# Kernel optimization log

Hardware: AMD Instinct MI355X
Metric: run time of the kernel (lower is better)

The kernel has to match this reference:

```python
import jax, jax.numpy as jnp
import numpy as np

N_QUBITS = 14
N_LOCAL = 3
VQC_DEPTH = 6
BATCH = 512
NLOC = 2 ** N_LOCAL            # 8 = Hermitian dimension
NOFF = NLOC * (NLOC - 1) // 2  # 28 off-diagonal params
_ROWS, _COLS = np.tril_indices(NLOC, -1)  # row-major order matches the torch nested loop


def _make_hermitian(a, b, d):
    # Faithful to create_Hermitian: h[i,j]=A[k]+iB[k] for j<i (row-major over i=1..N-1),
    # h[i-1,i-1]=D[i] for i=1..N-1 (D[0] unused, last diag 0), then H = h + h^H.
    tri = jnp.zeros((NLOC, NLOC), jnp.complex64).at[_ROWS, _COLS].set(a + 1j * b)
    diag = jnp.concatenate([d[1:], jnp.zeros(1, d.dtype)]).astype(jnp.complex64)
    h = tri + jnp.diag(diag)
    return h + h.conj().T


def _apply_ry(state, angle, wire):
    # state: (B, 2, 2, ..., 2); angle: scalar (shared) or (B,) per-sample
    half = 0.5 * angle
    c, s = jnp.cos(half), jnp.sin(half)
    if jnp.ndim(angle) == 1:
        bshape = (angle.shape[0],) + (1,) * (N_QUBITS - 1)
        c, s = c.reshape(bshape), s.reshape(bshape)
    s0 = jnp.take(state, 0, axis=wire + 1)
    s1 = jnp.take(state, 1, axis=wire + 1)
    return jnp.stack([c * s0 - s * s1, s * s0 + c * s1], axis=wire + 1)


def _apply_cnot(state, ctrl):
    # CNOT with target = ctrl + 1 (the only pattern used by entangling_layer)
    ax = ctrl + 1
    s0 = jnp.take(state, 0, axis=ax)
    s1 = jnp.take(state, 1, axis=ax)
    # after removing the control axis, the target axis sits at position ax
    s1 = jnp.flip(s1, axis=ax)
    return jnp.stack([s0, s1], axis=ax)


def _circuit(X, theta, H):
    B = X.shape[0]
    # Hadamard layer applied to |0...0> yields the uniform superposition
    amp = 1.0 / np.sqrt(2.0 ** N_QUBITS)
    state = jnp.full((B,) + (2,) * N_QUBITS, amp, dtype=jnp.complex64)
    for w in range(N_QUBITS):
        state = _apply_ry(state, X[:, w], w)
    for k in range(VQC_DEPTH):
        for i in range(0, N_QUBITS - 1, 2):
            state = _apply_cnot(state, i)
        for i in range(1, N_QUBITS - 1, 2):
            state = _apply_cnot(state, i)
        for w in range(N_QUBITS):
            state = _apply_ry(state, theta[k, w], w)
    exps = []
    for q in range(N_QUBITS):
        wires = [(q + j) % N_QUBITS for j in range(N_LOCAL)]
        psi = jnp.moveaxis(state, [w + 1 for w in wires], list(range(1, N_LOCAL + 1)))
        psi = psi.reshape(B, NLOC, -1)  # (B, 8, 2^(n-3))
        e = jnp.einsum('bir,ij,bjr->b', psi.conj(), H[q], psi).real
        exps.append(e)
    return jnp.stack(exps, axis=1).astype(jnp.float32)  # (B, n_qubits)


def setup_inputs() -> dict:
    key = jax.random.key(0)
    k = jax.random.split(key, 5)
    X = jax.random.normal(k[0], (BATCH, N_QUBITS), jnp.float32)
    theta = 0.01 * jax.random.normal(k[1], (VQC_DEPTH, N_QUBITS), jnp.float32)
    A = 2.0 * jax.random.normal(k[2], (N_QUBITS, NOFF), jnp.float32)
    Bp = 2.0 * jax.random.normal(k[3], (N_QUBITS, NOFF), jnp.float32)
    D = 2.0 * jax.random.normal(k[4], (N_QUBITS, NLOC), jnp.float32)
    return {"X": X, "theta": theta, "A": A, "B": Bp, "D": D}


def reference(X, theta, A, B, D):
    H = jax.vmap(_make_hermitian)(A, B, D)  # (n_qubits, 8, 8) complex64
    q_out = _circuit(X, theta, H)
    return q_out[:, :2]
```

## Files before the change

kernel.cpp:

```cpp
#include <hip/hip_runtime.h>
#include <math.h>

#define NQ 14
#define NSTATE (1 << 14)
#define DEPTH  6
#define NT     1024

typedef float v2f __attribute__((ext_vector_type(2)));

__device__ __forceinline__ int swz(int n) { return n ^ ((n >> 4) & 28); }

__device__ __forceinline__ int sigma(int n) {
    int m = n ^ ((n & 0x1554) >> 1);
    return m ^ ((m & 0x2AAA) >> 1);
}

__device__ __forceinline__ v2f pkmul_cc(v2f a, v2f cs) {
    v2f d;
    asm("v_pk_mul_f32 %0, %1, %2 op_sel:[0,0] op_sel_hi:[1,0]"
        : "=v"(d) : "v"(a), "v"(cs));
    return d;
}
__device__ __forceinline__ v2f pkmul_ss(v2f a, v2f cs) {
    v2f d;
    asm("v_pk_mul_f32 %0, %1, %2 op_sel:[0,1] op_sel_hi:[1,1]"
        : "=v"(d) : "v"(a), "v"(cs));
    return d;
}
__device__ __forceinline__ v2f pkfma_cc(v2f a, v2f cs, v2f acc) {
    v2f d;
    asm("v_pk_fma_f32 %0, %1, %2, %3 op_sel:[0,0,0] op_sel_hi:[1,0,1]"
        : "=v"(d) : "v"(a), "v"(cs), "v"(acc));
    return d;
}
__device__ __forceinline__ v2f pkfma_nss(v2f a, v2f cs, v2f acc) {
    v2f d;
    asm("v_pk_fma_f32 %0, %1, %2, %3 op_sel:[0,1,0] op_sel_hi:[1,1,1] neg_lo:[0,1,0] neg_hi:[0,1,0]"
        : "=v"(d) : "v"(a), "v"(cs), "v"(acc));
    return d;
}
__device__ __forceinline__ v2f pkfma_sw(v2f a, v2f cs, v2f acc) {
    v2f d;
    asm("v_pk_fma_f32 %0, %1, %2, %3 op_sel:[1,1,0] op_sel_hi:[0,1,1] neg_lo:[0,1,0] neg_hi:[0,0,0]"
        : "=v"(d) : "v"(a), "v"(cs), "v"(acc));
    return d;
}
__device__ __forceinline__ v2f pkfma(v2f a, v2f bb, v2f acc) {
    v2f d;
    asm("v_pk_fma_f32 %0, %1, %2, %3"
        : "=v"(d) : "v"(a), "v"(bb), "v"(acc));
    return d;
}

__device__ __forceinline__ void ry_pk0(float (&p)[16], v2f cs) {
#pragma unroll
    for (int j = 0; j < 8; ++j) {
        v2f v = *(v2f*)&p[2 * j];
        *(v2f*)&p[2 * j] = pkfma_sw(v, cs, pkmul_cc(v, cs));
    }
}
template <int JB>
__device__ __forceinline__ void ry_pkN(float (&p)[16], v2f cs) {
#pragma unroll
    for (int j = 0; j < 8; ++j) {
        if (!((j >> (JB - 1)) & 1)) {
            const int j1 = j | (1 << (JB - 1));
            v2f a0 = *(v2f*)&p[2 * j], a1 = *(v2f*)&p[2 * j1];
            *(v2f*)&p[2 * j]  = pkfma_nss(a1, cs, pkmul_cc(a0, cs));
            *(v2f*)&p[2 * j1] = pkfma_cc(a1, cs, pkmul_ss(a0, cs));
        }
    }
}
__device__ __forceinline__ void ry4_pk(float (&p)[16], float2 q0, float2 q1,
                                       float2 q2, float2 q3) {
    v2f c0, c1, c2, c3;
    c0.x = q0.x; c0.y = q0.y;
    c1.x = q1.x; c1.y = q1.y;
    c2.x = q2.x; c2.y = q2.y;
    c3.x = q3.x; c3.y = q3.y;
    ry_pk0(p, c0);
    ry_pkN<1>(p, c1);
    ry_pkN<2>(p, c2);
    ry_pkN<3>(p, c3);
}

template <int CTRL>
__device__ __forceinline__ void ry_dpp_pk(float (&p)[16], float c, float sg) {
    v2f cs; cs.x = c; cs.y = 0.0f;
    v2f sgv; sgv.x = sg; sgv.y = sg;
#pragma unroll
    for (int j = 0; j < 8; ++j) {
        v2f pt;
        pt.x = __int_as_float(__builtin_amdgcn_update_dpp(
            0, __float_as_int(p[2 * j]), CTRL, 0xF, 0xF, true));
        pt.y = __int_as_float(__builtin_amdgcn_update_dpp(
            0, __float_as_int(p[2 * j + 1]), CTRL, 0xF, 0xF, true));
        v2f v = *(v2f*)&p[2 * j];
        *(v2f*)&p[2 * j] = pkfma(pt, sgv, pkmul_cc(v, cs));
    }
}

template <int C1, int C2>
__device__ __forceinline__ void ry_dpp2_pk(float (&p)[16], float c, float sg) {
    v2f cs; cs.x = c; cs.y = 0.0f;
    v2f sgv; sgv.x = sg; sgv.y = sg;
#pragma unroll
    for (int j = 0; j < 8; ++j) {
        v2f pt;
        int ax = __builtin_amdgcn_update_dpp(
            0, __float_as_int(p[2 * j]), C1, 0xF, 0xF, true);
        pt.x = __int_as_float(__builtin_amdgcn_update_dpp(
            0, ax, C2, 0xF, 0xF, true));
        int ay = __builtin_amdgcn_update_dpp(
            0, __float_as_int(p[2 * j + 1]), C1, 0xF, 0xF, true);
        pt.y = __int_as_float(__builtin_amdgcn_update_dpp(
            0, ay, C2, 0xF, 0xF, true));
        v2f v = *(v2f*)&p[2 * j];
        *(v2f*)&p[2 * j] = pkfma(pt, sgv, pkmul_cc(v, cs));
    }
}

__global__ __launch_bounds__(NT, 4)
void vqc_kernel(const float* __restrict__ X,
                const float* __restrict__ TH,
                const float* __restrict__ A,
                const float* __restrict__ Bc,
                const float* __restrict__ D,
                float* __restrict__ out)
{
    __shared__ __align__(16) float st[NSTATE];
    __shared__ float2 tb[DEPTH * NQ];
    __shared__ float2 xf[NQ];
    __shared__ float  red[2 * (NT / 64)];

    const int t = threadIdx.x;
    const int b = blockIdx.x;

    if (t < DEPTH * NQ) {
        float s, c;
        __sincosf(0.5f * TH[t], &s, &c);
        tb[t] = make_float2(c, s);
    } else if (t < DEPTH * NQ + NQ) {
        const int j = t - DEPTH * NQ;
        float s, c;
        __sincosf(0.5f * X[b * NQ + (13 - j)], &s, &c);
        xf[j] = make_float2(c - s, c + s);
    }
    __syncthreads();

    {
        const int mt = sigma(t << 4);
        float sh = 1.0f / 128.0f;
#pragma unroll
        for (int j = 4; j < 14; ++j) {
            float2 f = xf[j];
            sh *= ((mt >> j) & 1) ? f.y : f.x;
        }
        float fa[4], fb[4];
#pragma unroll
        for (int j = 0; j < 4; ++j) {
            float2 f = xf[j];
            const int mj = (mt >> j) & 1;
            fa[j] = mj ? f.y : f.x;
            fb[j] = mj ? f.x : f.y;
        }
        float p[16];
#pragma unroll
        for (int i = 0; i < 16; ++i) {
            const int sl = sigma(i);
            float v = sh;
            v *= (sl & 1)        ? fb[0] : fa[0];
            v *= ((sl >> 1) & 1) ? fb[1] : fa[1];
            v *= ((sl >> 2) & 1) ? fb[2] : fa[2];
            v *= ((sl >> 3) & 1) ? fb[3] : fa[3];
            p[i] = v;
        }
        ry4_pk(p, tb[13], tb[12], tb[11], tb[10]);
        float2 w9 = tb[9], w8 = tb[8];
        const float sg9 = (t & 1) ? w9.y : -w9.y;
        const float sg8 = (t & 2) ? w8.y : -w8.y;
        ry_dpp_pk<0xB1>(p, w9.x, sg9);
        ry_dpp_pk<0x4E>(p, w8.x, sg8);
        const int wb = swz(t << 4);
#pragma unroll
        for (int g = 0; g < 4; ++g)
            *(float4*)&st[wb ^ (g << 2)] =
                make_float4(p[4 * g], p[4 * g + 1], p[4 * g + 2], p[4 * g + 3]);
    }
    __syncthreads();

    for (int k = 0; k < DEPTH; ++k) {
        const float2* tbk = tb + k * NQ;

        if (k > 0) {
            const int rb = swz(sigma(t << 4) & ~15) ^ ((t & 1) * 12);
            float tmpf[16];
#pragma unroll
            for (int g = 0; g < 4; ++g)
                *(float4*)&tmpf[g * 4] = *(const float4*)&st[rb ^ (g << 2)];
            float p[16];
#pragma unroll
            for (int i = 0; i < 16; ++i) {
                const int i0 = i & 1, i1 = (i >> 1) & 1, i2 = (i >> 2) & 1, i3 = (i >> 3) & 1;
                const int s = (i0 ^ i1 ^ i2) | ((i1 ^ i2) << 1) | ((i2 ^ i3) << 2) | (i3 << 3);
                p[i] = tmpf[s];
            }
            __syncthreads();
            ry4_pk(p, tbk[13], tbk[12], tbk[11], tbk[10]);
            float2 w9 = tbk[9], w8 = tbk[8];
            const float sg9 = (t & 1) ? w9.y : -w9.y;
            const float sg8 = (t & 2) ? w8.y : -w8.y;
            ry_dpp_pk<0xB1>(p, w9.x, sg9);
            ry_dpp_pk<0x4E>(p, w8.x, sg8);
            const int wb = swz(t << 4);
#pragma unroll
            for (int g = 0; g < 4; ++g)
                *(float4*)&st[wb ^ (g << 2)] =
                    make_float4(p[4 * g], p[4 * g + 1], p[4 * g + 2], p[4 * g + 3]);
            __syncthreads();
        }

        {
            const int raw = ((t >> 4) & 3) | (((t >> 6) & 15) << 2)
                          | ((t & 3) << 6) | (((t >> 2) & 3) << 8);
            const int base2 = swz(raw);
            float p[16];
#pragma unroll
            for (int i = 0; i < 16; ++i) p[i] = st[base2 + (i << 10)];
            ry4_pk(p, tbk[3], tbk[2], tbk[1], tbk[0]);
            float2 w7 = tbk[7], w6 = tbk[6], w5 = tbk[5], w4 = tbk[4];
            const float sg7 = (t & 1) ? w7.y : -w7.y;
            const float sg6 = (t & 2) ? w6.y : -w6.y;
            const float sg5 = (t & 4) ? w5.y : -w5.y;
            const float sg4 = (t & 8) ? w4.y : -w4.y;
            ry_dpp_pk<0xB1>(p, w7.x, sg7);
            ry_dpp_pk<0x4E>(p, w6.x, sg6);
            ry_dpp2_pk<0x1B, 0x141>(p, w5.x, sg5);
            ry_dpp2_pk<0x141, 0x140>(p, w4.x, sg4);
#pragma unroll
            for (int i = 0; i < 16; ++i) st[base2 + (i << 10)] = p[i];
            __syncthreads();
        }
    }

    float e[2];
#pragma unroll
    for (int q = 0; q < 2; ++q) {
        const int shift = 11 - q;
        float dg[8];
#pragma unroll
        for (int i = 0; i < 7; ++i) dg[i] = 2.0f * D[q * 8 + i + 1];
        dg[7] = 0.0f;
        float acc = 0.0f;
        const int lowmask = (1 << shift) - 1;
        for (int r = t; r < NSTATE / 8; r += NT) {
            const int base = ((r >> shift) << (shift + 3)) | (r & lowmask);
            float ps[8];
#pragma unroll
            for (int i = 0; i < 8; ++i) ps[i] = st[swz(base + (i << shift))];
#pragma unroll
            for (int i = 0; i < 8; ++i) acc += dg[i] * ps[i] * ps[i];
            int kk = 0;
#pragma unroll
            for (int i = 1; i < 8; ++i)
#pragma unroll
                for (int j = 0; j < i; ++j, ++kk)
                    acc += 2.0f * A[q * 28 + kk] * ps[i] * ps[j];
        }
        e[q] = acc;
    }

    float v0 = e[0], v1 = e[1];
#pragma unroll
    for (int o = 32; o > 0; o >>= 1) {
        v0 += __shfl_down(v0, o);
        v1 += __shfl_down(v1, o);
    }
    if ((t & 63) == 0) {
        red[(t >> 6) * 2]     = v0;
        red[(t >> 6) * 2 + 1] = v1;
    }
    __syncthreads();
    if (t == 0) {
        float s0 = 0.0f, s1 = 0.0f;
#pragma unroll
        for (int i = 0; i < NT / 64; ++i) { s0 += red[i * 2]; s1 += red[i * 2 + 1]; }
        out[b * 2 + 0] = s0;
        out[b * 2 + 1] = s1;
    }
}

extern "C" void kernel_launch(void* const* d_in, const int* in_sizes, int n_in,
                              void* d_out, int out_size, void* d_ws, size_t ws_size,
                              hipStream_t stream) {
    const float* X  = (const float*)d_in[0];
    const float* TH = (const float*)d_in[1];
    const float* A  = (const float*)d_in[2];
    const float* Bc = (const float*)d_in[3];
    const float* D  = (const float*)d_in[4];
    float* out = (float*)d_out;
    vqc_kernel<<<512, NT, 0, stream>>>(X, TH, A, Bc, D, out);
}
```

Baseline: 49.11 us.

## Restructure per-layer shared-memory passes with permuted state layout and merged phases

Reworks the depth loop so each layer does two LDS round-trips instead of three, folding the CNOT permutation into a precomputed permuted index map (Pd/sigma) for the read. The initial state build is merged into the k==0 iteration, so that shared-memory pass and its barrier disappear. The expectation-value phase uses the new physical layout with fixed unrolled indexing. The new mapping adds index math and may cause LDS bank conflicts on the scalar strided accesses.

```diff
diff --git a/kernel.cpp b/kernel.cpp
--- a/kernel.cpp
+++ b/kernel.cpp
@@ -13,6 +13,11 @@
 __device__ __forceinline__ int sigma(int n) {
     int m = n ^ ((n & 0x1554) >> 1);
     return m ^ ((m & 0x2AAA) >> 1);
+}
+
+__device__ __forceinline__ int Pd(int m) {
+    return ((m >> 4) & 15) | (((m >> 8) & 3) << 4) | (((m >> 10) & 15) << 6)
+         | ((m & 15) << 10);
 }
 
 __device__ __forceinline__ v2f pkmul_cc(v2f a, v2f cs) {
@@ -148,116 +153,105 @@
     }
     __syncthreads();
 
-    {
-        const int mt = sigma(t << 4);
-        float sh = 1.0f / 128.0f;
-#pragma unroll
-        for (int j = 4; j < 14; ++j) {
-            float2 f = xf[j];
-            sh *= ((mt >> j) & 1) ? f.y : f.x;
-        }
-        float fa[4], fb[4];
-#pragma unroll
-        for (int j = 0; j < 4; ++j) {
-            float2 f = xf[j];
-            const int mj = (mt >> j) & 1;
-            fa[j] = mj ? f.y : f.x;
-            fb[j] = mj ? f.x : f.y;
-        }
-        float p[16];
-#pragma unroll
-        for (int i = 0; i < 16; ++i) {
-            const int sl = sigma(i);
-            float v = sh;
-            v *= (sl & 1)        ? fb[0] : fa[0];
-            v *= ((sl >> 1) & 1) ? fb[1] : fa[1];
-            v *= ((sl >> 2) & 1) ? fb[2] : fa[2];
-            v *= ((sl >> 3) & 1) ? fb[3] : fa[3];
-            p[i] = v;
-        }
-        ry4_pk(p, tb[13], tb[12], tb[11], tb[10]);
-        float2 w9 = tb[9], w8 = tb[8];
-        const float sg9 = (t & 1) ? w9.y : -w9.y;
-        const float sg8 = (t & 2) ? w8.y : -w8.y;
-        ry_dpp_pk<0xB1>(p, w9.x, sg9);
-        ry_dpp_pk<0x4E>(p, w8.x, sg8);
-        const int wb = swz(t << 4);
-#pragma unroll
-        for (int g = 0; g < 4; ++g)
-            *(float4*)&st[wb ^ (g << 2)] =
-                make_float4(p[4 * g], p[4 * g + 1], p[4 * g + 2], p[4 * g + 3]);
-    }
-    __syncthreads();
+    const int nbase = (((t >> 4) & 3) << 4) | (((t >> 6) & 15) << 6)
+                    | ((t & 15) << 10);
+    const int msrc  = sigma(nbase);
+    const int rbase = swz(Pd(msrc));
+    const int wbase = swz(Pd(nbase));
+    const int pbase = swz(((t & 15) << 4) | (((t >> 6) & 3) << 8)
+                        | (((t >> 4) & 3) << 10) | (((t >> 8) & 3) << 12));
 
     for (int k = 0; k < DEPTH; ++k) {
         const float2* tbk = tb + k * NQ;
-
-        if (k > 0) {
-            const int rb = swz(sigma(t << 4) & ~15) ^ ((t & 1) * 12);
-            float tmpf[16];
-#pragma unroll
-            for (int g = 0; g < 4; ++g)
-                *(float4*)&tmpf[g * 4] = *(const float4*)&st[rb ^ (g << 2)];
-            float p[16];
+        float p[16];
+
+        if (k == 0) {
+            float sh = 1.0f / 128.0f;
+#pragma unroll
+            for (int j = 4; j < 14; ++j) {
+                float2 f = xf[j];
+                sh *= ((msrc >> j) & 1) ? f.y : f.x;
+            }
+            float fa[4], fb[4];
+#pragma unroll
+            for (int j = 0; j < 4; ++j) {
+                float2 f = xf[j];
+                const int mj = (msrc >> j) & 1;
+                fa[j] = mj ? f.y : f.x;
+                fb[j] = mj ? f.x : f.y;
+            }
 #pragma unroll
             for (int i = 0; i < 16; ++i) {
-                const int i0 = i & 1, i1 = (i >> 1) & 1, i2 = (i >> 2) & 1, i3 = (i >> 3) & 1;
-                const int s = (i0 ^ i1 ^ i2) | ((i1 ^ i2) << 1) | ((i2 ^ i3) << 2) | (i3 << 3);
-                p[i] = tmpf[s];
-            }
+                const int sl = sigma(i);
+                float v = sh;
+                v *= (sl & 1)        ? fb[0] : fa[0];
+                v *= ((sl >> 1) & 1) ? fb[1] : fa[1];
+                v *= ((sl >> 2) & 1) ? fb[2] : fa[2];
+                v *= ((sl >> 3) & 1) ? fb[3] : fa[3];
+                p[i] = v;
+            }
+        } else {
+#pragma unroll
+            for (int i = 0; i < 16; ++i)
+                p[i] = st[rbase ^ (sigma(i) << 10)];
             __syncthreads();
-            ry4_pk(p, tbk[13], tbk[12], tbk[11], tbk[10]);
-            float2 w9 = tbk[9], w8 = tbk[8];
-            const float sg9 = (t & 1) ? w9.y : -w9.y;
-            const float sg8 = (t & 2) ? w8.y : -w8.y;
-            ry_dpp_pk<0xB1>(p, w9.x, sg9);
-            ry_dpp_pk<0x4E>(p, w8.x, sg8);
-            const int wb = swz(t << 4);
-#pragma unroll
-            for (int g = 0; g < 4; ++g)
-                *(float4*)&st[wb ^ (g << 2)] =
-                    make_float4(p[4 * g], p[4 * g + 1], p[4 * g + 2], p[4 * g + 3]);
-            __syncthreads();
-        }
-
+        }
+        ry4_pk(p, tbk[13], tbk[12], tbk[11], tbk[10]);
         {
-            const int raw = ((t >> 4) & 3) | (((t >> 6) & 15) << 2)
-                          | ((t & 3) << 6) | (((t >> 2) & 3) << 8);
-            const int base2 = swz(raw);
-            float p[16];
-#pragma unroll
-            for (int i = 0; i < 16; ++i) p[i] = st[base2 + (i << 10)];
-            ry4_pk(p, tbk[3], tbk[2], tbk[1], tbk[0]);
-            float2 w7 = tbk[7], w6 = tbk[6], w5 = tbk[5], w4 = tbk[4];
-            const float sg7 = (t & 1) ? w7.y : -w7.y;
-            const float sg6 = (t & 2) ? w6.y : -w6.y;
-            const float sg5 = (t & 4) ? w5.y : -w5.y;
-            const float sg4 = (t & 8) ? w4.y : -w4.y;
-            ry_dpp_pk<0xB1>(p, w7.x, sg7);
-            ry_dpp_pk<0x4E>(p, w6.x, sg6);
-            ry_dpp2_pk<0x1B, 0x141>(p, w5.x, sg5);
-            ry_dpp2_pk<0x141, 0x140>(p, w4.x, sg4);
-#pragma unroll
-            for (int i = 0; i < 16; ++i) st[base2 + (i << 10)] = p[i];
-            __syncthreads();
-        }
+            float2 u3 = tbk[3], u2 = tbk[2], u1 = tbk[1], u0 = tbk[0];
+            const float s3 = (t & 1) ? u3.y : -u3.y;
+            const float s2 = (t & 2) ? u2.y : -u2.y;
+            const float s1 = (t & 4) ? u1.y : -u1.y;
+            const float s0 = (t & 8) ? u0.y : -u0.y;
+            ry_dpp_pk<0xB1>(p, u3.x, s3);
+            ry_dpp_pk<0x4E>(p, u2.x, s2);
+            ry_dpp2_pk<0x1B, 0x141>(p, u1.x, s1);
+            ry_dpp2_pk<0x141, 0x140>(p, u0.x, s0);
+        }
+#pragma unroll
+        for (int i = 0; i < 16; ++i) st[wbase | (i << 10)] = p[i];
+        __syncthreads();
+
+#pragma unroll
+        for (int g = 0; g < 4; ++g)
+            *(float4*)&p[4 * g] = *(const float4*)&st[pbase + 4 * g];
+        ry4_pk(p, tbk[9], tbk[8], tbk[7], tbk[6]);
+        {
+            float2 u5 = tbk[5], u4 = tbk[4];
+            const float s5 = (t & 1) ? u5.y : -u5.y;
+            const float s4 = (t & 2) ? u4.y : -u4.y;
+            ry_dpp_pk<0xB1>(p, u5.x, s5);
+            ry_dpp_pk<0x4E>(p, u4.x, s4);
+        }
+#pragma unroll
+        for (int g = 0; g < 4; ++g)
+            *(float4*)&st[pbase + 4 * g] = *(const float4*)&p[4 * g];
+        __syncthreads();
     }
 
     float e[2];
 #pragma unroll
     for (int q = 0; q < 2; ++q) {
-        const int shift = 11 - q;
         float dg[8];
 #pragma unroll
         for (int i = 0; i < 7; ++i) dg[i] = 2.0f * D[q * 8 + i + 1];
         dg[7] = 0.0f;
         float acc = 0.0f;
-        const int lowmask = (1 << shift) - 1;
-        for (int r = t; r < NSTATE / 8; r += NT) {
-            const int base = ((r >> shift) << (shift + 3)) | (r & lowmask);
+#pragma unroll
+        for (int half = 0; half < 2; ++half) {
+            const int r = t + half * NT;
+            const int lbase = (q == 0)
+                ? ((r & 127) | ((r >> 7) << 10))
+                : ((r & 63) | (((r >> 6) & 1) << 9) | ((r >> 7) << 10));
+            const int ebase = swz(lbase);
             float ps[8];
 #pragma unroll
-            for (int i = 0; i < 8; ++i) ps[i] = st[swz(base + (i << shift))];
+            for (int i = 0; i < 8; ++i) {
+                const int off = (q == 0)
+                    ? (((i & 1) << 7) | (((i >> 1) & 1) << 8) | (((i >> 2) & 1) << 9))
+                    : (((i & 1) << 6) | (((i >> 1) & 1) << 7) | (((i >> 2) & 1) << 8));
+                ps[i] = st[ebase ^ swz(off)];
+            }
 #pragma unroll
             for (int i = 0; i < 8; ++i) acc += dg[i] * ps[i] * ps[i];
             int kk = 0;
```

Result: slower. 61.99 us (+26.2%).
